# Kernel optimization log

Hardware: AMD Instinct MI355X
Metric: run time of the kernel (lower is better)

Reference implementation:

```python
import jax, jax.numpy as jnp
import numpy as np

B, N, D = 2, 16384, 512
H = 256          # gated-attention hidden dim
C, K = 4, 8      # num classes, descriptions per class
EPS = 1e-12


def _l2norm(x):
    return x / jnp.clip(jnp.linalg.norm(x, axis=-1, keepdims=True), EPS)


def setup_inputs() -> dict:
    key = jax.random.key(0)
    ks = jax.random.split(key, 12)
    inp = {
        'x_s': jax.random.normal(ks[0], (B, N, D), jnp.float32),
        'coord_s': jax.random.uniform(ks[1], (B, N, 2), jnp.float32),
        'x_l': jax.random.normal(ks[2], (B, N, D), jnp.float32),
        'coord_l': jax.random.uniform(ks[3], (B, N, 2), jnp.float32),
        # visual_proj: Linear(D, D), stored as [in, out] (apply x @ W + b)
        'W_proj': jax.random.normal(ks[4], (D, D), jnp.float32) / np.sqrt(D),
        'b_proj': jnp.zeros((D,), jnp.float32),
        # frozen, L2-normalized text description features [C, K, D]
        'desc_feats': _l2norm(jax.random.normal(ks[5], (C, K, D), jnp.float32)),
        # GatedAttentionPooling params ([in, out] layout)
        'Wv': jax.random.normal(ks[6], (D, H), jnp.float32) / np.sqrt(D),
        'bv': jnp.zeros((H,), jnp.float32),
        'Wu': jax.random.normal(ks[7], (D, H), jnp.float32) / np.sqrt(D),
        'bu': jnp.zeros((H,), jnp.float32),
        'w_attn': jax.random.normal(ks[8], (H,), jnp.float32) / np.sqrt(H),
        'b_attn': jnp.zeros((), jnp.float32),
    }
    return inp


def _class_scores(xp, desc_feats):
    # xp: [B,N,D] normalized projected patches; desc_feats: [C,K,D]
    scale = desc_feats.shape[-1] ** (-0.5)
    sim = jnp.einsum('bnd,ckd->bnck', xp, desc_feats) * scale  # [B,N,C,K]
    attn = jax.nn.softmax(sim, axis=-1)
    # scores_c = <xp, attn @ desc_c> collapsed without materializing [B,N,C,D]
    return jnp.einsum('bnck,ckd,bnd->bnc', attn, desc_feats, xp)  # [B,N,C]


def _gated_pool(feats, Wv, bv, Wu, bu, w_attn, b_attn):
    # feats: [B,N,D]
    A_V = jnp.tanh(feats @ Wv + bv)                 # [B,N,H]
    A_U = jax.nn.sigmoid(feats @ Wu + bu)           # [B,N,H]
    A = (A_V * A_U) @ w_attn + b_attn               # [B,N]
    A = jax.nn.softmax(A, axis=1)
    return jnp.einsum('bn,bnd->bd', A, feats)       # [B,D]


def reference(x_s, coord_s, x_l, coord_l, W_proj, b_proj, desc_feats,
              Wv, bv, Wu, bu, w_attn, b_attn):
    # coords are unused by the compute path (kept for signature fidelity)
    x_s_proj = _l2norm(_l2norm(x_s) @ W_proj + b_proj)
    x_l_proj = _l2norm(_l2norm(x_l) @ W_proj + b_proj)

    class_scores_s = _class_scores(x_s_proj, desc_feats)  # [B,N,C]
    class_scores_l = _class_scores(x_l_proj, desc_feats)

    slide_s = _l2norm(_gated_pool(x_s_proj, Wv, bv, Wu, bu, w_attn, b_attn))
    slide_l = _l2norm(_gated_pool(x_l_proj, Wv, bv, Wu, bu, w_attn, b_attn))

    # text_features_low: per-class max over descriptions, L2-normalized
    text_feats = _l2norm(jnp.max(desc_feats, axis=1))      # [C,D]

    logits = slide_s @ text_feats.T + slide_l @ text_feats.T  # [B,C]
    Y_prob = jax.nn.softmax(logits, axis=1)
    Y_hat = jnp.argmax(Y_prob, axis=1)
    return Y_prob, Y_hat, class_scores_s, class_scores_l
```

## Files before the change

### kernel.cpp

```cpp
#include <hip/hip_runtime.h>
#include <math.h>

#define B_ 2
#define N_ 16384
#define D_ 512
#define C_ 4
#define K_ 8
#define ROWS (B_*N_)
#define ROWS2 (2*ROWS)
#define EPS_ 1e-12f

typedef unsigned short u16;
typedef unsigned int u32;
using short8  = __attribute__((ext_vector_type(8))) short;
using float4v = __attribute__((ext_vector_type(4))) float;

__device__ __forceinline__ u16 f2bf(float f) {
    union { float f; u32 u; } v; v.f = f;
    u32 r = v.u + 0x7fffu + ((v.u >> 16) & 1u);
    return (u16)(r >> 16);
}
__device__ __forceinline__ u32 pack2(float a, float b) {
    return (u32)f2bf(a) | ((u32)f2bf(b) << 16);
}
__device__ __forceinline__ float bf2f(u16 h) {
    union { u32 u; float f; } v; v.u = ((u32)h) << 16;
    return v.f;
}
__device__ __forceinline__ float fsigmoid(float x) { return 1.0f / (1.0f + __expf(-x)); }
__device__ __forceinline__ float ftanh(float x)    { return 1.0f - 2.0f / (__expf(2.0f * x) + 1.0f); }

__device__ __forceinline__ void load_lds16(const u16* g, u16* l) {
    __builtin_amdgcn_global_load_lds(
        (const __attribute__((address_space(1))) u32*)g,
        (__attribute__((address_space(3))) u32*)l, 16, 0, 0);
}
__device__ __forceinline__ void stage_rows8(const u16* gtile, u16* ldsTile, int g, int lane) {
    int rg = lane >> 3;
    int c  = (lane & 7) ^ rg;
    load_lds16(gtile + (size_t)(g * 8 + rg) * 512 + c * 8, ldsTile + g * 512);
}
#define AFRAG(lds, R, c) (*(const short8*)&(lds)[(R) * 64 + (((c) ^ ((R) & 7)) * 8)])

__global__ __launch_bounds__(256) void prep_weights_kernel(
    const float* __restrict__ Wp, const float* __restrict__ Wv, const float* __restrict__ Wu,
    const float* __restrict__ bv, const float* __restrict__ bu, const float* __restrict__ desc,
    u16* __restrict__ WpT, u16* __restrict__ WvuT, float* __restrict__ bvu,
    u16* __restrict__ descF)
{
    int idx = blockIdx.x * 256 + threadIdx.x;
    int n = idx >> 9, k = idx & 511;
    WpT[idx] = f2bf(Wp[k * 512 + n]);
    int tile = n >> 4, pair = tile >> 1, half = tile & 1, h = pair * 16 + (n & 15);
    WvuT[idx] = f2bf(half ? Wu[k * 256 + h] : Wv[k * 256 + h]);
    if (idx < 512) {
        int tl = idx >> 4, pr = tl >> 1, hf = tl & 1, hh = pr * 16 + (idx & 15);
        bvu[idx] = hf ? bu[hh] : bv[hh];
    }
    if (idx < 16384) {
        int j = idx & 7, l = (idx >> 3) & 63, g = (idx >> 9) & 1, kt = idx >> 10;
        descF[idx] = f2bf(desc[(size_t)(g * 16 + (l & 15)) * 512 + kt * 32 + (l >> 4) * 8 + j]);
    }
}

__global__ __launch_bounds__(256) void rownorm_cast_kernel(
    const float* __restrict__ x_s, const float* __restrict__ x_l, u16* __restrict__ xn)
{
    int wave = threadIdx.x >> 6, lane = threadIdx.x & 63;
    size_t row = (size_t)blockIdx.x * 4 + wave;
    const float* xr = (row < (size_t)ROWS) ? (x_s + row * D_)
                                           : (x_l + (row - ROWS) * D_);
    float4 a = *(const float4*)&xr[lane * 8];
    float4 b = *(const float4*)&xr[lane * 8 + 4];
    float s = a.x*a.x + a.y*a.y + a.z*a.z + a.w*a.w
            + b.x*b.x + b.y*b.y + b.z*b.z + b.w*b.w;
#pragma unroll
    for (int off = 32; off; off >>= 1) s += __shfl_xor(s, off, 64);
    float inv = 1.0f / fmaxf(sqrtf(s), EPS_);
    uint4 o;
    o.x = pack2(a.x * inv, a.y * inv);
    o.y = pack2(a.z * inv, a.w * inv);
    o.z = pack2(b.x * inv, b.y * inv);
    o.w = pack2(b.z * inv, b.w * inv);
    *(uint4*)&xn[row * D_ + lane * 8] = o;
}

__global__ __launch_bounds__(256, 2) void gemm_bias_kernel(
    const u16* __restrict__ A, const u16* __restrict__ Bt,
    const float* __restrict__ bias, u16* __restrict__ C, float* __restrict__ sumsq)
{
    __shared__ u16 ldsA[128 * 64];
    __shared__ u16 ldsB[128 * 64];
    int t = threadIdx.x, wave = t >> 6, lane = t & 63;
    int lr = lane & 15, lq = lane >> 4;
    int wm = wave >> 1, wn = wave & 1;
    int M0 = blockIdx.y * 128, N0 = blockIdx.x * 128;

    float4v acc[4][4];
#pragma unroll
    for (int i = 0; i < 4; ++i)
#pragma unroll
        for (int j = 0; j < 4; ++j)
#pragma unroll
            for (int r = 0; r < 4; ++r) acc[i][j][r] = 0.f;

    for (int k0 = 0; k0 < 512; k0 += 64) {
        const u16* Ab = A  + (size_t)M0 * 512 + k0;
        const u16* Bb = Bt + (size_t)N0 * 512 + k0;
#pragma unroll
        for (int s = 0; s < 4; ++s) stage_rows8(Ab, ldsA, wave * 4 + s, lane);
#pragma unroll
        for (int s = 0; s < 4; ++s) stage_rows8(Bb, ldsB, wave * 4 + s, lane);
        __syncthreads();
#pragma unroll
        for (int kt = 0; kt < 2; ++kt) {
            short8 af[4], bfr[4];
#pragma unroll
            for (int i = 0; i < 4; ++i)
                af[i] = AFRAG(ldsA, wm * 64 + i * 16 + lr, kt * 4 + lq);
#pragma unroll
            for (int j = 0; j < 4; ++j)
                bfr[j] = AFRAG(ldsB, wn * 64 + j * 16 + lr, kt * 4 + lq);
#pragma unroll
            for (int i = 0; i < 4; ++i)
#pragma unroll
                for (int j = 0; j < 4; ++j)
                    acc[i][j] = __builtin_amdgcn_mfma_f32_16x16x32_bf16(bfr[j], af[i], acc[i][j], 0, 0, 0);
        }
        __syncthreads();
    }

    float4 b4[4];
#pragma unroll
    for (int j = 0; j < 4; ++j)
        b4[j] = *(const float4*)&bias[N0 + wn * 64 + j * 16 + lq * 4];
#pragma unroll
    for (int i = 0; i < 4; ++i) {
        int m = M0 + wm * 64 + i * 16 + lr;
        u16* crow = C + (size_t)m * 512;
        float sq = 0.f;
#pragma unroll
        for (int j = 0; j < 4; ++j) {
            int nb = N0 + wn * 64 + j * 16 + lq * 4;
            float v0 = acc[i][j][0] + b4[j].x, v1 = acc[i][j][1] + b4[j].y;
            float v2 = acc[i][j][2] + b4[j].z, v3 = acc[i][j][3] + b4[j].w;
            u16 h0 = f2bf(v0), h1 = f2bf(v1), h2 = f2bf(v2), h3 = f2bf(v3);
            uint2 o;
            o.x = (u32)h0 | ((u32)h1 << 16);
            o.y = (u32)h2 | ((u32)h3 << 16);
            *(uint2*)&crow[nb] = o;
            float q0 = bf2f(h0), q1 = bf2f(h1), q2 = bf2f(h2), q3 = bf2f(h3);
            sq += q0*q0 + q1*q1 + q2*q2 + q3*q3;
        }
        sq += __shfl_xor(sq, 16, 64);
        sq += __shfl_xor(sq, 32, 64);
        if (lq == 0) atomicAdd(&sumsq[m], sq);
    }
}

__global__ __launch_bounds__(256, 2) void gatecls_kernel(
    const u16* __restrict__ A, const u16* __restrict__ Bt,
    const u16* __restrict__ descF,
    const float* __restrict__ bvu, const float* __restrict__ w_attn,
    const float* __restrict__ sumsq, float* __restrict__ Araw4,
    float* __restrict__ out10)
{
    __shared__ u16 ldsA[128 * 64];
    __shared__ u16 ldsB[128 * 64];
    int t = threadIdx.x, wave = t >> 6, lane = t & 63;
    int lr = lane & 15, lq = lane >> 4;
    int wm = wave >> 1, wn = wave & 1;
    int M0 = blockIdx.y * 128, N0 = blockIdx.x * 128;
    const bool doCls = (blockIdx.x == 0);

    float4v acc[4][4];
    float4v accS[2][2];
#pragma unroll
    for (int i = 0; i < 4; ++i)
#pragma unroll
        for (int j = 0; j < 4; ++j)
#pragma unroll
            for (int r = 0; r < 4; ++r) acc[i][j][r] = 0.f;
#pragma unroll
    for (int h = 0; h < 2; ++h)
#pragma unroll
        for (int r = 0; r < 4; ++r) { accS[h][0][r] = 0.f; accS[h][1][r] = 0.f; }

    for (int k0 = 0; k0 < 512; k0 += 64) {
        const u16* Ab = A  + (size_t)M0 * 512 + k0;
        const u16* Bb = Bt + (size_t)N0 * 512 + k0;
#pragma unroll
        for (int s = 0; s < 4; ++s) stage_rows8(Ab, ldsA, wave * 4 + s, lane);
#pragma unroll
        for (int s = 0; s < 4; ++s) stage_rows8(Bb, ldsB, wave * 4 + s, lane);
        __syncthreads();
#pragma unroll
        for (int kt = 0; kt < 2; ++kt) {
            if (doCls) {
                int ktg = (k0 >> 5) + kt;
                short8 d0 = *(const short8*)&descF[(ktg * 2 + 0) * 512 + lane * 8];
                short8 d1 = *(const short8*)&descF[(ktg * 2 + 1) * 512 + lane * 8];
#pragma unroll
                for (int h = 0; h < 2; ++h) {
                    short8 afc = AFRAG(ldsA, wave * 32 + h * 16 + lr, kt * 4 + lq);
                    accS[h][0] = __builtin_amdgcn_mfma_f32_16x16x32_bf16(afc, d0, accS[h][0], 0, 0, 0);
                    accS[h][1] = __builtin_amdgcn_mfma_f32_16x16x32_bf16(afc, d1, accS[h][1], 0, 0, 0);
                }
            }
            short8 af[4], bfr[4];
#pragma unroll
            for (int i = 0; i < 4; ++i)
                af[i] = AFRAG(ldsA, wm * 64 + i * 16 + lr, kt * 4 + lq);
#pragma unroll
            for (int j = 0; j < 4; ++j)
                bfr[j] = AFRAG(ldsB, wn * 64 + j * 16 + lr, kt * 4 + lq);
#pragma unroll
            for (int i = 0; i < 4; ++i)
#pragma unroll
                for (int j = 0; j < 4; ++j)
                    acc[i][j] = __builtin_amdgcn_mfma_f32_16x16x32_bf16(bfr[j], af[i], acc[i][j], 0, 0, 0);
        }
        __syncthreads();
    }

    if (doCls) {
        const float scale = 0.04419417382415922f;
        int side = (M0 >= ROWS) ? 1 : 0;
        float* cls = out10 + (size_t)side * ((size_t)ROWS * 4);
#pragma unroll
        for (int h = 0; h < 2; ++h) {
#pragma unroll
            for (int r = 0; r < 4; ++r) {
                int grow = M0 + wave * 32 + h * 16 + lq * 4 + r;
                float iv = 1.0f / fmaxf(sqrtf(sumsq[grow]), EPS_);
                float sv0 = accS[h][0][r] * iv, sv1 = accS[h][1][r] * iv;
#pragma unroll
                for (int g = 0; g < 2; ++g) {
                    float s = g ? sv1 : sv0;
                    float ts = s * scale;
                    float mx = ts;
                    mx = fmaxf(mx, __shfl_xor(mx, 1, 64));
                    mx = fmaxf(mx, __shfl_xor(mx, 2, 64));
                    mx = fmaxf(mx, __shfl_xor(mx, 4, 64));
                    float e = __expf(ts - mx);
                    float num = e * s, den = e;
                    num += __shfl_xor(num, 1, 64); den += __shfl_xor(den, 1, 64);
                    num += __shfl_xor(num, 2, 64); den += __shfl_xor(den, 2, 64);
                    num += __shfl_xor(num, 4, 64); den += __shfl_xor(den, 4, 64);
                    if ((lr & 7) == 0) {
                        int c = g * 2 + ((lr >> 3) & 1);
                        cls[(size_t)(grow - side * ROWS) * 4 + c] = num / den;
                    }
                }
            }
        }
    }

    int colbase = N0 + wn * 64;
    int hbase = colbase >> 1;
    float4 bv4[2], bu4[2], w4[2];
#pragma unroll
    for (int p = 0; p < 2; ++p) {
        int nv = colbase + p * 32 + lq * 4;
        bv4[p] = *(const float4*)&bvu[nv];
        bu4[p] = *(const float4*)&bvu[nv + 16];
        w4[p]  = *(const float4*)&w_attn[hbase + p * 16 + lq * 4];
    }
    float* redA = (float*)ldsA;
#pragma unroll
    for (int i = 0; i < 4; ++i) {
        int rloc = wm * 64 + i * 16 + lr;
        float iv = 1.0f / fmaxf(sqrtf(sumsq[M0 + rloc]), EPS_);
        float part = 0.f;
#pragma unroll
        for (int p = 0; p < 2; ++p) {
#pragma unroll
            for (int r = 0; r < 4; ++r) {
                float v = acc[i][2 * p][r] * iv + (&bv4[p].x)[r];
                float u = acc[i][2 * p + 1][r] * iv + (&bu4[p].x)[r];
                part += ftanh(v) * (&w4[p].x)[r] * fsigmoid(u);
            }
        }
        part += __shfl_xor(part, 16, 64);
        part += __shfl_xor(part, 32, 64);
        if (lq == 0) redA[wn * 128 + rloc] = part;
    }
    __syncthreads();
    if (t < 128)
        Araw4[(size_t)blockIdx.x * ROWS2 + M0 + t] = redA[t] + redA[128 + t];
}

__global__ __launch_bounds__(256) void areduce_kernel(
    float* __restrict__ Araw4, float* __restrict__ part)
{
    __shared__ float red[256];
    int t = threadIdx.x, g = blockIdx.y;
    size_t i0 = (size_t)g * N_ + blockIdx.x * 512 + t * 2;
    float v0 = Araw4[i0]     + Araw4[i0 + ROWS2]     + Araw4[i0 + 2*ROWS2]     + Araw4[i0 + 3*ROWS2];
    float v1 = Araw4[i0 + 1] + Araw4[i0 + 1 + ROWS2] + Araw4[i0 + 1 + 2*ROWS2] + Araw4[i0 + 1 + 3*ROWS2];
    *(float2*)&Araw4[i0] = make_float2(v0, v1);
    red[t] = fmaxf(v0, v1); __syncthreads();
    for (int s = 128; s; s >>= 1) { if (t < s) red[t] = fmaxf(red[t], red[t + s]); __syncthreads(); }
    float m = red[0]; __syncthreads();
    red[t] = __expf(v0 - m) + __expf(v1 - m); __syncthreads();
    for (int s = 128; s; s >>= 1) { if (t < s) red[t] += red[t + s]; __syncthreads(); }
    if (t == 0) {
        int pi = g * 32 + blockIdx.x;
        part[pi * 2] = m;
        part[pi * 2 + 1] = red[0];
    }
}

__global__ __launch_bounds__(128) void acombine_kernel(
    const float* __restrict__ part, float* __restrict__ mg)
{
    int t = threadIdx.x;
    int g = t >> 5, j = t & 31;
    float m = part[(g * 32 + j) * 2];
    float s = part[(g * 32 + j) * 2 + 1];
    float mm = m;
#pragma unroll
    for (int off = 1; off < 32; off <<= 1) mm = fmaxf(mm, __shfl_xor(mm, off, 64));
    float sc = s * __expf(m - mm);
#pragma unroll
    for (int off = 1; off < 32; off <<= 1) sc += __shfl_xor(sc, off, 64);
    if (j == 0) {
        mg[g * 2] = mm;
        mg[g * 2 + 1] = 1.0f / sc;
    }
}

__global__ __launch_bounds__(256) void pool_kernel(
    const float* __restrict__ Araw, const float* __restrict__ sumsq,
    const float* __restrict__ mg, const u16* __restrict__ xpraw,
    float* __restrict__ slideAll)
{
    __shared__ float lds[4][512];
    int t = threadIdx.x, wave = t >> 6, lane = t & 63;
    int g = blockIdx.y;
    float m = mg[g * 2], is = mg[g * 2 + 1];
    size_t row0 = (size_t)g * N_ + (size_t)blockIdx.x * 256 + wave;
    float a[8] = {};
    for (int r = 0; r < 64; ++r) {
        size_t row = row0 + r * 4;
        float iv = 1.0f / fmaxf(sqrtf(sumsq[row]), EPS_);
        float av = __expf(Araw[row] - m) * is * iv;
        uint4 pk = *(const uint4*)&xpraw[row * D_ + lane * 8];
        a[0] += av * bf2f((u16)pk.x); a[1] += av * bf2f((u16)(pk.x >> 16));
        a[2] += av * bf2f((u16)pk.y); a[3] += av * bf2f((u16)(pk.y >> 16));
        a[4] += av * bf2f((u16)pk.z); a[5] += av * bf2f((u16)(pk.z >> 16));
        a[6] += av * bf2f((u16)pk.w); a[7] += av * bf2f((u16)(pk.w >> 16));
    }
#pragma unroll
    for (int i = 0; i < 8; ++i) lds[wave][lane * 8 + i] = a[i];
    __syncthreads();
#pragma unroll
    for (int q = 0; q < 2; ++q) {
        int c = t * 2 + q;
        float s = lds[0][c] + lds[1][c] + lds[2][c] + lds[3][c];
        atomicAdd(&slideAll[(size_t)g * 512 + c], s);
    }
}

__global__ __launch_bounds__(512) void finalize_kernel(
    const float* __restrict__ slide_s, const float* __restrict__ slide_l,
    const float* __restrict__ desc, float* __restrict__ out)
{
    __shared__ float txt[4][512];
    __shared__ float ssn[2][512];
    __shared__ float sln[2][512];
    __shared__ float red[512];
    __shared__ float lg[8];
    int t = threadIdx.x;

    auto reduceSum = [&](float v) -> float {
        red[t] = v; __syncthreads();
        for (int s = 256; s; s >>= 1) { if (t < s) red[t] += red[t + s]; __syncthreads(); }
        float r = red[0]; __syncthreads();
        return r;
    };

    for (int c = 0; c < 4; ++c) {
        float m = -1e30f;
        for (int k = 0; k < 8; ++k) m = fmaxf(m, desc[((size_t)c * 8 + k) * 512 + t]);
        float ss = reduceSum(m * m);
        txt[c][t] = m / fmaxf(sqrtf(ss), EPS_);
    }
    for (int b = 0; b < 2; ++b) {
        float v = slide_s[b * 512 + t];
        float ss = reduceSum(v * v);
        ssn[b][t] = v / fmaxf(sqrtf(ss), EPS_);
        v = slide_l[b * 512 + t];
        ss = reduceSum(v * v);
        sln[b][t] = v / fmaxf(sqrtf(ss), EPS_);
    }
    __syncthreads();
    for (int b = 0; b < 2; ++b)
        for (int c = 0; c < 4; ++c) {
            float v = ssn[b][t] * txt[c][t] + sln[b][t] * txt[c][t];
            float s = reduceSum(v);
            if (t == 0) lg[b * 4 + c] = s;
        }
    __syncthreads();
    if (t < 2) {
        int b = t;
        float m = -1e30f;
        for (int c = 0; c < 4; ++c) m = fmaxf(m, lg[b * 4 + c]);
        float e[4]; float den = 0.f;
        for (int c = 0; c < 4; ++c) { e[c] = expf(lg[b * 4 + c] - m); den += e[c]; }
        int am = 0; float bm = -1.f;
        for (int c = 0; c < 4; ++c) {
            float pcl = e[c] / den;
            out[b * 4 + c] = pcl;
            if (pcl > bm) { bm = pcl; am = c; }
        }
        out[8 + b] = (float)am;
    }
}

extern "C" void kernel_launch(void* const* d_in, const int* in_sizes, int n_in,
                              void* d_out, int out_size, void* d_ws, size_t ws_size,
                              hipStream_t stream) {
    const float* x_s    = (const float*)d_in[0];
    const float* x_l    = (const float*)d_in[2];
    const float* W_proj = (const float*)d_in[4];
    const float* b_proj = (const float*)d_in[5];
    const float* desc   = (const float*)d_in[6];
    const float* Wv     = (const float*)d_in[7];
    const float* bv     = (const float*)d_in[8];
    const float* Wu     = (const float*)d_in[9];
    const float* bu     = (const float*)d_in[10];
    const float* w_attn = (const float*)d_in[11];
    float* out = (float*)d_out;

    char* w = (char*)d_ws;
    u16* xn        = (u16*)w;
    u16* xpraw     = (u16*)(w + 67108864);
    u16* WpT       = (u16*)(w + 134217728);
    u16* WvuT      = (u16*)(w + 134742016);
    u16* descF     = (u16*)(w + 135266304);
    float* bvu     = (float*)(w + 135299072);
    float* sumsq   = (float*)(w + 135301120);
    float* slideAll= (float*)(w + 135563264);
    float* Araw4   = (float*)(w + 135571456);
    float* part    = (float*)(w + 136620032);
    float* mg      = (float*)(w + 136621056);

    hipMemsetAsync(sumsq, 0, 262144 + 8192, stream);
    prep_weights_kernel<<<1024, 256, 0, stream>>>(W_proj, Wv, Wu, bv, bu, desc,
                                                  WpT, WvuT, bvu, descF);

    rownorm_cast_kernel<<<ROWS2 / 4, 256, 0, stream>>>(x_s, x_l, xn);
    gemm_bias_kernel<<<dim3(4, 512), 256, 0, stream>>>(xn, WpT, b_proj, xpraw, sumsq);
    gatecls_kernel<<<dim3(4, 512), 256, 0, stream>>>(xpraw, WvuT, descF, bvu, w_attn,
                                                     sumsq, Araw4, out + 10);
    areduce_kernel<<<dim3(32, 4), 256, 0, stream>>>(Araw4, part);
    acombine_kernel<<<1, 128, 0, stream>>>(part, mg);
    pool_kernel<<<dim3(64, 4), 256, 0, stream>>>(Araw4, sumsq, mg, xpraw, slideAll);
    finalize_kernel<<<1, 512, 0, stream>>>(slideAll, slideAll + 1024, desc, out);
}
```

Measured before the change: 352.1 us.

## Double-buffer A tiles, read pre-fragmented weights from global, swizzle block order

Weights are repacked in the prep kernel into an MFMA-fragment-ordered layout, so both GEMM kernels read B fragments straight from global/L2 and no longer stage B through LDS. The freed LDS holds a second A buffer, so the next K-slab of A is prefetched while the current one is consumed. A 1D grid with a block-index decode groups the column blocks of nearby row tiles to improve L2 reuse. The trade-off is more global/L2 traffic and latency on the B reads in exchange for less LDS staging and fewer stalls on A loads.

```diff
diff --git a/kernel.cpp b/kernel.cpp
--- a/kernel.cpp
+++ b/kernel.cpp
@@ -41,25 +41,28 @@
     load_lds16(gtile + (size_t)(g * 8 + rg) * 512 + c * 8, ldsTile + g * 512);
 }
 #define AFRAG(lds, R, c) (*(const short8*)&(lds)[(R) * 64 + (((c) ^ ((R) & 7)) * 8)])
+#define BFRAG(Bf, nf, ks, lane) (*(const short8*)&(Bf)[((size_t)((nf) * 16 + (ks)) << 9) + ((lane) << 3)])
 
 __global__ __launch_bounds__(256) void prep_weights_kernel(
     const float* __restrict__ Wp, const float* __restrict__ Wv, const float* __restrict__ Wu,
     const float* __restrict__ bv, const float* __restrict__ bu, const float* __restrict__ desc,
-    u16* __restrict__ WpT, u16* __restrict__ WvuT, float* __restrict__ bvu,
+    u16* __restrict__ WpF, u16* __restrict__ WvuF, float* __restrict__ bvu,
     u16* __restrict__ descF)
 {
     int idx = blockIdx.x * 256 + threadIdx.x;
-    int n = idx >> 9, k = idx & 511;
-    WpT[idx] = f2bf(Wp[k * 512 + n]);
-    int tile = n >> 4, pair = tile >> 1, half = tile & 1, h = pair * 16 + (n & 15);
-    WvuT[idx] = f2bf(half ? Wu[k * 256 + h] : Wv[k * 256 + h]);
+    int e = idx & 7, l = (idx >> 3) & 63, ks = (idx >> 9) & 15, nf = idx >> 13;
+    int k = ks * 32 + ((l >> 4) << 3) + e;
+    int n = (nf << 4) + (l & 15);
+    WpF[idx] = f2bf(Wp[(size_t)k * 512 + n]);
+    int half = nf & 1, h = (nf >> 1) * 16 + (l & 15);
+    WvuF[idx] = f2bf(half ? Wu[(size_t)k * 256 + h] : Wv[(size_t)k * 256 + h]);
     if (idx < 512) {
         int tl = idx >> 4, pr = tl >> 1, hf = tl & 1, hh = pr * 16 + (idx & 15);
         bvu[idx] = hf ? bu[hh] : bv[hh];
     }
     if (idx < 16384) {
-        int j = idx & 7, l = (idx >> 3) & 63, g = (idx >> 9) & 1, kt = idx >> 10;
-        descF[idx] = f2bf(desc[(size_t)(g * 16 + (l & 15)) * 512 + kt * 32 + (l >> 4) * 8 + j]);
+        int j = idx & 7, dl = (idx >> 3) & 63, g = (idx >> 9) & 1, kt = idx >> 10;
+        descF[idx] = f2bf(desc[(size_t)(g * 16 + (dl & 15)) * 512 + kt * 32 + (dl >> 4) * 8 + j]);
     }
 }
 
@@ -85,16 +88,22 @@
     *(uint4*)&xn[row * D_ + lane * 8] = o;
 }
 
+__device__ __forceinline__ void decode_mn(int d, int& M0, int& N0) {
+    int n = (d >> 3) & 3;
+    int m = (d & 7) | ((d >> 5) << 3);
+    M0 = m * 128; N0 = n * 128;
+}
+
 __global__ __launch_bounds__(256, 2) void gemm_bias_kernel(
-    const u16* __restrict__ A, const u16* __restrict__ Bt,
+    const u16* __restrict__ A, const u16* __restrict__ Bf,
     const float* __restrict__ bias, u16* __restrict__ C, float* __restrict__ sumsq)
 {
-    __shared__ u16 ldsA[128 * 64];
-    __shared__ u16 ldsB[128 * 64];
+    __shared__ u16 ldsA[2][128 * 64];
     int t = threadIdx.x, wave = t >> 6, lane = t & 63;
     int lr = lane & 15, lq = lane >> 4;
     int wm = wave >> 1, wn = wave & 1;
-    int M0 = blockIdx.y * 128, N0 = blockIdx.x * 128;
+    int M0, N0; decode_mn(blockIdx.x, M0, N0);
+    const u16* Arow = A + (size_t)M0 * 512;
 
     float4v acc[4][4];
 #pragma unroll
@@ -104,23 +113,27 @@
 #pragma unroll
             for (int r = 0; r < 4; ++r) acc[i][j][r] = 0.f;
 
-    for (int k0 = 0; k0 < 512; k0 += 64) {
-        const u16* Ab = A  + (size_t)M0 * 512 + k0;
-        const u16* Bb = Bt + (size_t)N0 * 512 + k0;
-#pragma unroll
-        for (int s = 0; s < 4; ++s) stage_rows8(Ab, ldsA, wave * 4 + s, lane);
-#pragma unroll
-        for (int s = 0; s < 4; ++s) stage_rows8(Bb, ldsB, wave * 4 + s, lane);
-        __syncthreads();
+#pragma unroll
+    for (int s = 0; s < 4; ++s) stage_rows8(Arow, ldsA[0], wave * 4 + s, lane);
+    __syncthreads();
+
+    for (int tt = 0; tt < 8; ++tt) {
+        int cur = tt & 1;
+        if (tt < 7) {
+            const u16* Ab = Arow + (tt + 1) * 64;
+#pragma unroll
+            for (int s = 0; s < 4; ++s) stage_rows8(Ab, ldsA[cur ^ 1], wave * 4 + s, lane);
+        }
 #pragma unroll
         for (int kt = 0; kt < 2; ++kt) {
+            int ks = tt * 2 + kt;
             short8 af[4], bfr[4];
 #pragma unroll
             for (int i = 0; i < 4; ++i)
-                af[i] = AFRAG(ldsA, wm * 64 + i * 16 + lr, kt * 4 + lq);
+                af[i] = AFRAG(ldsA[cur], wm * 64 + i * 16 + lr, kt * 4 + lq);
 #pragma unroll
             for (int j = 0; j < 4; ++j)
-                bfr[j] = AFRAG(ldsB, wn * 64 + j * 16 + lr, kt * 4 + lq);
+                bfr[j] = BFRAG(Bf, (N0 >> 4) + wn * 4 + j, ks, lane);
 #pragma unroll
             for (int i = 0; i < 4; ++i)
 #pragma unroll
@@ -159,19 +172,20 @@
 }
 
 __global__ __launch_bounds__(256, 2) void gatecls_kernel(
-    const u16* __restrict__ A, const u16* __restrict__ Bt,
+    const u16* __restrict__ A, const u16* __restrict__ Bf,
     const u16* __restrict__ descF,
     const float* __restrict__ bvu, const float* __restrict__ w_attn,
     const float* __restrict__ sumsq, float* __restrict__ Araw4,
     float* __restrict__ out10)
 {
-    __shared__ u16 ldsA[128 * 64];
-    __shared__ u16 ldsB[128 * 64];
+    __shared__ u16 ldsA[2][128 * 64];
     int t = threadIdx.x, wave = t >> 6, lane = t & 63;
     int lr = lane & 15, lq = lane >> 4;
     int wm = wave >> 1, wn = wave & 1;
-    int M0 = blockIdx.y * 128, N0 = blockIdx.x * 128;
-    const bool doCls = (blockIdx.x == 0);
+    int M0, N0; decode_mn(blockIdx.x, M0, N0);
+    const int nblk = (N0 >> 7);
+    const bool doCls = (nblk == 0);
+    const u16* Arow = A + (size_t)M0 * 512;
 
     float4v acc[4][4];
     float4v accS[2][2];
@@ -186,23 +200,26 @@
 #pragma unroll
         for (int r = 0; r < 4; ++r) { accS[h][0][r] = 0.f; accS[h][1][r] = 0.f; }
 
-    for (int k0 = 0; k0 < 512; k0 += 64) {
-        const u16* Ab = A  + (size_t)M0 * 512 + k0;
-        const u16* Bb = Bt + (size_t)N0 * 512 + k0;
-#pragma unroll
-        for (int s = 0; s < 4; ++s) stage_rows8(Ab, ldsA, wave * 4 + s, lane);
-#pragma unroll
-        for (int s = 0; s < 4; ++s) stage_rows8(Bb, ldsB, wave * 4 + s, lane);
-        __syncthreads();
+#pragma unroll
+    for (int s = 0; s < 4; ++s) stage_rows8(Arow, ldsA[0], wave * 4 + s, lane);
+    __syncthreads();
+
+    for (int tt = 0; tt < 8; ++tt) {
+        int cur = tt & 1;
+        if (tt < 7) {
+            const u16* Ab = Arow + (tt + 1) * 64;
+#pragma unroll
+            for (int s = 0; s < 4; ++s) stage_rows8(Ab, ldsA[cur ^ 1], wave * 4 + s, lane);
+        }
 #pragma unroll
         for (int kt = 0; kt < 2; ++kt) {
+            int ks = tt * 2 + kt;
             if (doCls) {
-                int ktg = (k0 >> 5) + kt;
-                short8 d0 = *(const short8*)&descF[(ktg * 2 + 0) * 512 + lane * 8];
-                short8 d1 = *(const short8*)&descF[(ktg * 2 + 1) * 512 + lane * 8];
+                short8 d0 = *(const short8*)&descF[(ks * 2 + 0) * 512 + lane * 8];
+                short8 d1 = *(const short8*)&descF[(ks * 2 + 1) * 512 + lane * 8];
 #pragma unroll
                 for (int h = 0; h < 2; ++h) {
-                    short8 afc = AFRAG(ldsA, wave * 32 + h * 16 + lr, kt * 4 + lq);
+                    short8 afc = AFRAG(ldsA[cur], wave * 32 + h * 16 + lr, kt * 4 + lq);
                     accS[h][0] = __builtin_amdgcn_mfma_f32_16x16x32_bf16(afc, d0, accS[h][0], 0, 0, 0);
                     accS[h][1] = __builtin_amdgcn_mfma_f32_16x16x32_bf16(afc, d1, accS[h][1], 0, 0, 0);
                 }
@@ -210,10 +227,10 @@
             short8 af[4], bfr[4];
 #pragma unroll
             for (int i = 0; i < 4; ++i)
-                af[i] = AFRAG(ldsA, wm * 64 + i * 16 + lr, kt * 4 + lq);
+                af[i] = AFRAG(ldsA[cur], wm * 64 + i * 16 + lr, kt * 4 + lq);
 #pragma unroll
             for (int j = 0; j < 4; ++j)
-                bfr[j] = AFRAG(ldsB, wn * 64 + j * 16 + lr, kt * 4 + lq);
+                bfr[j] = BFRAG(Bf, (N0 >> 4) + wn * 4 + j, ks, lane);
 #pragma unroll
             for (int i = 0; i < 4; ++i)
 #pragma unroll
@@ -266,7 +283,7 @@
         bu4[p] = *(const float4*)&bvu[nv + 16];
         w4[p]  = *(const float4*)&w_attn[hbase + p * 16 + lq * 4];
     }
-    float* redA = (float*)ldsA;
+    float* redA = (float*)&ldsA[0][0];
 #pragma unroll
     for (int i = 0; i < 4; ++i) {
         int rloc = wm * 64 + i * 16 + lr;
@@ -287,7 +304,7 @@
     }
     __syncthreads();
     if (t < 128)
-        Araw4[(size_t)blockIdx.x * ROWS2 + M0 + t] = redA[t] + redA[128 + t];
+        Araw4[(size_t)nblk * ROWS2 + M0 + t] = redA[t] + redA[128 + t];
 }
 
 __global__ __launch_bounds__(256) void areduce_kernel(
@@ -436,8 +453,8 @@
     char* w = (char*)d_ws;
     u16* xn        = (u16*)w;
     u16* xpraw     = (u16*)(w + 67108864);
-    u16* WpT       = (u16*)(w + 134217728);
-    u16* WvuT      = (u16*)(w + 134742016);
+    u16* WpF       = (u16*)(w + 134217728);
+    u16* WvuF      = (u16*)(w + 134742016);
     u16* descF     = (u16*)(w + 135266304);
     float* bvu     = (float*)(w + 135299072);
     float* sumsq   = (float*)(w + 135301120);
@@ -448,12 +465,12 @@
 
     hipMemsetAsync(sumsq, 0, 262144 + 8192, stream);
     prep_weights_kernel<<<1024, 256, 0, stream>>>(W_proj, Wv, Wu, bv, bu, desc,
-                                                  WpT, WvuT, bvu, descF);
+                                                  WpF, WvuF, bvu, descF);
 
     rownorm_cast_kernel<<<ROWS2 / 4, 256, 0, stream>>>(x_s, x_l, xn);
-    gemm_bias_kernel<<<dim3(4, 512), 256, 0, stream>>>(xn, WpT, b_proj, xpraw, sumsq);
-    gatecls_kernel<<<dim3(4, 512), 256, 0, stream>>>(xpraw, WvuT, descF, bvu, w_attn,
-                                                     sumsq, Araw4, out + 10);
+    gemm_bias_kernel<<<2048, 256, 0, stream>>>(xn, WpF, b_proj, xpraw, sumsq);
+    gatecls_kernel<<<2048, 256, 0, stream>>>(xpraw, WvuF, descF, bvu, w_attn,
+                                             sumsq, Araw4, out + 10);
     areduce_kernel<<<dim3(32, 4), 256, 0, stream>>>(Araw4, part);
     acombine_kernel<<<1, 128, 0, stream>>>(part, mg);
     pool_kernel<<<dim3(64, 4), 256, 0, stream>>>(Araw4, sumsq, mg, xpraw, slideAll);
```

After: 341.3 us. -3.1%, faster.
